# Kernel tuning notes

Hardware: AMD Instinct MI355X
Metric: run time of the kernel (lower is better)

Reference implementation:

```python
import jax, jax.numpy as jnp
import numpy as np

THRESHOLD_IOU = 0.8  # forward default in the original module


def setup_inputs() -> dict:
    key = jax.random.key(0)
    k1, k2, k3, k4 = jax.random.split(key, 4)
    N = M = 16
    H = W = 768
    # Binary masks (the original zeroes pixels to 0.0 and tests >0 via torch.where)
    masks_a = (jax.random.uniform(k1, (N, H, W)) > 0.6).astype(jnp.float32)
    masks_b = (jax.random.uniform(k2, (M, H, W)) > 0.6).astype(jnp.float32)
    # Make a few masks identical across labels so the IoU>threshold (suppression)
    # branch is exercised, not just the partial-overlap zeroing branch.
    masks_b = masks_b.at[:4].set(masks_a[:4])
    scores_a = jax.random.uniform(k3, (N,))
    scores_b = jax.random.uniform(k4, (M,))
    return {"masks_a": masks_a, "masks_b": masks_b,
            "scores_a": scores_a, "scores_b": scores_b}


def _overlap_filter(masks_a, masks_b, scores_a, scores_b, thr):
    # Sequential pairwise IoU + overlap zeroing, faithful to the original
    # nested product(enumerate(masks), enumerate(other_masks)) loop order
    # (i outer, j inner), where each pair sees masks already modified by
    # earlier pairs. Pruning ("keep") is applied after the loop; here it is
    # represented with static shapes as keep flags + zeroed-out rows.
    N, H, W = masks_a.shape
    M = masks_b.shape[0]
    P = H * W
    A0 = masks_a.reshape(N, P)
    B0 = masks_b.reshape(M, P)

    def body(carry, k):
        A, B, fi, fj = carry
        i = k // M
        j = k % M
        a = A[i]  # [P]
        b = B[j]  # [P]
        abin = a > 0
        bbin = b > 0
        inter = abin & bbin
        inter_sum = jnp.sum(inter.astype(jnp.float32))
        union_sum = jnp.sum((abin | bbin).astype(jnp.float32))
        iou = inter_sum / jnp.maximum(union_sum, 1.0)
        a_wins = scores_a[i] > scores_b[j]
        suppress = iou > thr                 # mark whole loser mask for removal
        zero_case = (iou > 0) & ~suppress    # zero overlapped pixels of loser
        b_new = jnp.where(zero_case & a_wins & inter, 0.0, b)
        a_new = jnp.where(zero_case & (~a_wins) & inter, 0.0, a)
        A = A.at[i].set(a_new)
        B = B.at[j].set(b_new)
        fj = fj.at[j].set(fj[j] | (suppress & a_wins))
        fi = fi.at[i].set(fi[i] | (suppress & ~a_wins))
        return (A, B, fi, fj), None

    fi0 = jnp.zeros(N, dtype=bool)
    fj0 = jnp.zeros(M, dtype=bool)
    (A, B, fi, fj), _ = jax.lax.scan(body, (A0, B0, fi0, fj0), jnp.arange(N * M))
    keep_a = ~fi
    keep_b = ~fj
    A = jnp.where(keep_a[:, None], A, 0.0)
    B = jnp.where(keep_b[:, None], B, 0.0)
    return A.reshape(N, H, W), B.reshape(M, H, W), keep_a, keep_b


def reference(masks_a, masks_b, scores_a, scores_b):
    return _overlap_filter(masks_a, masks_b, scores_a, scores_b, THRESHOLD_IOU)
```

## Files before the change

### kernel.cpp

```cpp
#include <hip/hip_runtime.h>
#include <stdint.h>

#define NM 16
#define HW_P 589824
#define WPM 18432
#define U8PM 9216
#define F4PM 147456
#define F4PT 2359296
#define PT 512
#define NG 8
#define U8PT 18

typedef unsigned long long u64;


__device__ __forceinline__ uint32_t spread4(uint32_t x) {
    uint32_t t = (x | (x << 12)) & 0x000F000Fu;
    t = (t | (t << 6)) & 0x03030303u;
    t = (t | (t << 3)) & 0x11111111u;
    return t;
}

__global__ __launch_bounds__(256) void binarize_kernel(
    const float* __restrict__ ma, const float* __restrict__ mb,
    uint32_t* __restrict__ bitsA, uint32_t* __restrict__ bitsB)
{
    int g = blockIdx.x * 256 + threadIdx.x;
    int tensor = (g >= F4PT);
    int lg = tensor ? (g - F4PT) : g;
    const float* src = tensor ? mb : ma;
    float4 v = ((const float4*)src)[lg];
    unsigned long long q0 = __ballot(v.x > 0.0f);
    unsigned long long q1 = __ballot(v.y > 0.0f);
    unsigned long long q2 = __ballot(v.z > 0.0f);
    unsigned long long q3 = __ballot(v.w > 0.0f);
    int lane = threadIdx.x & 63;
    if (lane < 8) {
        uint32_t wd = spread4((uint32_t)(q0 >> (8 * lane)) & 0xFFu)
                    | (spread4((uint32_t)(q1 >> (8 * lane)) & 0xFFu) << 1)
                    | (spread4((uint32_t)(q2 >> (8 * lane)) & 0xFFu) << 2)
                    | (spread4((uint32_t)(q3 >> (8 * lane)) & 0xFFu) << 3);
        uint32_t* bits = tensor ? bitsB : bitsA;
        bits[((lg & ~63) >> 3) + lane] = wd;
    }
}

__global__ __launch_bounds__(PT, 2) void pipeline_kernel(
    const float* __restrict__ sa, const float* __restrict__ sb,
    uint32_t* bitsA, uint32_t* bitsB, int* meta, u64* msg)
{
    int* flagsA = meta + 32;
    int* flagsB = meta + 48;
    unsigned* cons = (unsigned*)(meta + 64);
    unsigned* prodflag = (unsigned*)(meta + 96);

    const int g = blockIdx.x;
    const int tid = threadIdx.x;
    const int wave = tid >> 6, lane = tid & 63;
    const int c0 = 2 * g, c1 = 2 * g + 1;

    __shared__ int part[2][8][4];
    __shared__ unsigned smeta_s;

    u64* A8 = (u64*)bitsA;
    u64* B8 = (u64*)bitsB;

    u64 a[U8PT], b0[U8PT], b1[U8PT];
    int par = 0;

    int v0 = 0, v1 = 0;
#pragma unroll
    for (int w = 0; w < U8PT; ++w) {
        b0[w] = B8[(size_t)c0 * U8PM + tid + PT * w];
        b1[w] = B8[(size_t)c1 * U8PM + tid + PT * w];
        v0 += __popcll(b0[w]);
        v1 += __popcll(b1[w]);
    }
#pragma unroll
    for (int off = 32; off >= 1; off >>= 1) {
        v0 += __shfl_xor(v0, off); v1 += __shfl_xor(v1, off);
    }
    if (lane == 0) { part[par][wave][0] = v0; part[par][wave][1] = v1; }
    __syncthreads();
    int pcb0 = 0, pcb1 = 0;
#pragma unroll
    for (int w = 0; w < 8; ++w) { pcb0 += part[par][w][0]; pcb1 += part[par][w][1]; }
    par ^= 1;
    float sb0 = sb[c0], sb1 = sb[c1];
    int fb0 = 0, fb1 = 0;

    for (int t = 0; t < NM; ++t) {
        if (g > 0 && tid == 0) {
            unsigned v;
            while (!(v = __hip_atomic_load(&prodflag[(g - 1) * 16 + t],
                                           __ATOMIC_RELAXED, __HIP_MEMORY_SCOPE_AGENT)))
                __builtin_amdgcn_s_sleep(1);
            smeta_s = v;
        }
        if (g < NG - 1 && t >= 2 && tid == 64) {
            while (__hip_atomic_load(&cons[g], __ATOMIC_RELAXED,
                                     __HIP_MEMORY_SCOPE_AGENT) < (unsigned)(t - 1))
                __builtin_amdgcn_s_sleep(1);
        }
        __syncthreads();

        int pca, fa;
        if (g == 0) {
#pragma unroll
            for (int w = 0; w < U8PT; ++w)
                a[w] = A8[(size_t)t * U8PM + tid + PT * w];
            fa = 0; pca = 0;
        } else {
            unsigned v = smeta_s;
            pca = (int)((v >> 1) & 0xFFFFFu);
            fa  = (int)((v >> 21) & 1u);
            const u64* slot_in = msg + (size_t)((g - 1) * 2 + (t & 1)) * U8PM;
#pragma unroll
            for (int w = 0; w < U8PT; ++w)
                a[w] = __hip_atomic_load(&slot_in[tid + PT * w],
                                         __ATOMIC_RELAXED, __HIP_MEMORY_SCOPE_AGENT);
        }

        int i0 = 0, i1 = 0, it = 0, ip = 0;
#pragma unroll
        for (int w = 0; w < U8PT; ++w) {
            u64 ab0 = a[w] & b0[w];
            i0 += __popcll(ab0);
            i1 += __popcll(a[w] & b1[w]);
            it += __popcll(ab0 & b1[w]);
        }
        if (g == 0) {
#pragma unroll
            for (int w = 0; w < U8PT; ++w) ip += __popcll(a[w]);
        }
#pragma unroll
        for (int off = 32; off >= 1; off >>= 1) {
            i0 += __shfl_xor(i0, off); i1 += __shfl_xor(i1, off);
            it += __shfl_xor(it, off); ip += __shfl_xor(ip, off);
        }
        if (lane == 0) {
            part[par][wave][0] = i0; part[par][wave][1] = i1;
            part[par][wave][2] = it; part[par][wave][3] = ip;
        }
        __syncthreads();
        if (g > 0 && tid == 65)
            __hip_atomic_store(&cons[g - 1], (unsigned)(t + 1),
                               __ATOMIC_RELAXED, __HIP_MEMORY_SCOPE_AGENT);
        int I0 = 0, I1 = 0, T = 0, PC = 0;
#pragma unroll
        for (int w = 0; w < 8; ++w) {
            I0 += part[par][w][0]; I1 += part[par][w][1];
            T  += part[par][w][2]; PC += part[par][w][3];
        }
        par ^= 1;
        if (g == 0) pca = PC;

        float sai = sa[t];
        bool aupd = false;
        {
            int inter = I0;
            int uni = pca + pcb0 - inter;
            float iou = (float)inter / fmaxf((float)uni, 1.0f);
            bool aw = sai > sb0;
            if (iou > 0.8f) { if (aw) fb0 = 1; else fa = 1; }
            else if (inter > 0) {
                if (aw) {
                    pcb0 -= inter;
#pragma unroll
                    for (int w = 0; w < U8PT; ++w) b0[w] &= ~a[w];
                } else {
                    pca -= inter; aupd = true;
#pragma unroll
                    for (int w = 0; w < U8PT; ++w) a[w] &= ~b0[w];
                }
            }
        }
        {
            int inter = aupd ? (I1 - T) : I1;
            int uni = pca + pcb1 - inter;
            float iou = (float)inter / fmaxf((float)uni, 1.0f);
            bool aw = sai > sb1;
            if (iou > 0.8f) { if (aw) fb1 = 1; else fa = 1; }
            else if (inter > 0) {
                if (aw) {
                    pcb1 -= inter;
#pragma unroll
                    for (int w = 0; w < U8PT; ++w) b1[w] &= ~a[w];
                } else {
                    pca -= inter;
#pragma unroll
                    for (int w = 0; w < U8PT; ++w) a[w] &= ~b1[w];
                }
            }
        }

        if (g < NG - 1) {
            u64* slot_out = msg + (size_t)(g * 2 + (t & 1)) * U8PM;
#pragma unroll
            for (int w = 0; w < U8PT; ++w)
                __hip_atomic_store(&slot_out[tid + PT * w], a[w],
                                   __ATOMIC_RELAXED, __HIP_MEMORY_SCOPE_AGENT);
            __syncthreads();
            if (tid == 0)
                __hip_atomic_store(&prodflag[g * 16 + t],
                                   1u | ((unsigned)pca << 1) | ((unsigned)fa << 21),
                                   __ATOMIC_RELAXED, __HIP_MEMORY_SCOPE_AGENT);
        } else {
#pragma unroll
            for (int w = 0; w < U8PT; ++w)
                A8[(size_t)t * U8PM + tid + PT * w] = a[w];
            if (tid == 0) flagsA[t] = fa;
        }
    }
#pragma unroll
    for (int w = 0; w < U8PT; ++w) {
        B8[(size_t)c0 * U8PM + tid + PT * w] = b0[w];
        B8[(size_t)c1 * U8PM + tid + PT * w] = b1[w];
    }
    if (tid == 0) { flagsB[c0] = fb0; flagsB[c1] = fb1; }
}

__global__ __launch_bounds__(256) void expand_kernel(
    const uint32_t* __restrict__ bitsA, const uint32_t* __restrict__ bitsB,
    const int* __restrict__ meta, float* __restrict__ out)
{
    int g = blockIdx.x * 256 + threadIdx.x;
    int tensor = (g >= F4PT);
    int lg = tensor ? (g - F4PT) : g;
    const uint32_t* bits = tensor ? bitsB : bitsA;
    const int* flags = meta + (tensor ? 48 : 32);
    int m = lg / F4PM;
    bool keep = (flags[m] == 0);
    uint32_t wd = keep ? bits[lg >> 3] : 0u;
    int sh = (lg & 7) * 4;
    float4 o;
    o.x = ((wd >> (sh + 0)) & 1u) ? 1.0f : 0.0f;
    o.y = ((wd >> (sh + 1)) & 1u) ? 1.0f : 0.0f;
    o.z = ((wd >> (sh + 2)) & 1u) ? 1.0f : 0.0f;
    o.w = ((wd >> (sh + 3)) & 1u) ? 1.0f : 0.0f;
    ((float4*)out)[g] = o;
    if (g < 2 * NM) {
        const int* f = meta + 32;
        out[(size_t)2 * NM * HW_P + g] = f[g] ? 0.0f : 1.0f;
    }
}

extern "C" void kernel_launch(void* const* d_in, const int* in_sizes, int n_in,
                              void* d_out, int out_size, void* d_ws, size_t ws_size,
                              hipStream_t stream)
{
    const float* ma = (const float*)d_in[0];
    const float* mb = (const float*)d_in[1];
    const float* sa = (const float*)d_in[2];
    const float* sb = (const float*)d_in[3];
    float* out = (float*)d_out;
    char* ws = (char*)d_ws;

    uint32_t* bitsA = (uint32_t*)(ws);
    uint32_t* bitsB = (uint32_t*)(ws + 1179648);
    int* meta       = (int*)(ws + 2359296);
    u64* msg        = (u64*)(ws + 2360320);

    hipMemsetAsync(meta + 64, 0, 576, stream);

    binarize_kernel<<<18432, 256, 0, stream>>>(ma, mb, bitsA, bitsB);
    pipeline_kernel<<<NG, PT, 0, stream>>>(sa, sb, bitsA, bitsB, meta, msg);
    expand_kernel<<<18432, 256, 0, stream>>>(bitsA, bitsB, meta, out);
}
```

Before: 252.1 us.

## Deepen inter-block pipeline, drop memset, use nontemporal and 128-bit accesses

New measurement: 270.1 us. +7.1%, slower.

```diff
diff --git a/kernel.cpp b/kernel.cpp
--- a/kernel.cpp
+++ b/kernel.cpp
@@ -3,15 +3,14 @@
 
 #define NM 16
 #define HW_P 589824
-#define WPM 18432
 #define U8PM 9216
 #define F4PM 147456
 #define F4PT 2359296
 #define PT 512
 #define NG 8
-#define U8PT 18
 
 typedef unsigned long long u64;
+typedef float vf4 __attribute__((ext_vector_type(4)));
 
 
 __device__ __forceinline__ uint32_t spread4(uint32_t x) {
@@ -23,13 +22,15 @@
 
 __global__ __launch_bounds__(256) void binarize_kernel(
     const float* __restrict__ ma, const float* __restrict__ mb,
-    uint32_t* __restrict__ bitsA, uint32_t* __restrict__ bitsB)
+    uint32_t* __restrict__ bitsA, uint32_t* __restrict__ bitsB,
+    int* __restrict__ meta)
 {
+    if (blockIdx.x == 0) meta[threadIdx.x] = 0;
     int g = blockIdx.x * 256 + threadIdx.x;
     int tensor = (g >= F4PT);
     int lg = tensor ? (g - F4PT) : g;
     const float* src = tensor ? mb : ma;
-    float4 v = ((const float4*)src)[lg];
+    vf4 v = __builtin_nontemporal_load(((const vf4*)src) + lg);
     unsigned long long q0 = __ballot(v.x > 0.0f);
     unsigned long long q1 = __ballot(v.y > 0.0f);
     unsigned long long q2 = __ballot(v.z > 0.0f);
@@ -45,7 +46,7 @@
     }
 }
 
-__global__ __launch_bounds__(PT, 2) void pipeline_kernel(
+__global__ __launch_bounds__(PT, 1) void pipeline_kernel(
     const float* __restrict__ sa, const float* __restrict__ sb,
     uint32_t* bitsA, uint32_t* bitsB, int* meta, u64* msg)
 {
@@ -59,100 +60,108 @@
     const int wave = tid >> 6, lane = tid & 63;
     const int c0 = 2 * g, c1 = 2 * g + 1;
 
-    __shared__ int part[2][8][4];
+    __shared__ int part[8][4];
     __shared__ unsigned smeta_s;
 
     u64* A8 = (u64*)bitsA;
     u64* B8 = (u64*)bitsB;
 
-    u64 a[U8PT], b0[U8PT], b1[U8PT];
-    int par = 0;
-
+    u64 a[18], b0[18], b1[18];
+
+    const uint4* Bc0 = (const uint4*)(B8 + (size_t)c0 * U8PM);
+    const uint4* Bc1 = (const uint4*)(B8 + (size_t)c1 * U8PM);
+#pragma unroll
+    for (int w = 0; w < 9; ++w) {
+        uint4 q0 = Bc0[tid + PT * w];
+        uint4 q1 = Bc1[tid + PT * w];
+        b0[2 * w]     = ((u64)q0.y << 32) | q0.x;
+        b0[2 * w + 1] = ((u64)q0.w << 32) | q0.z;
+        b1[2 * w]     = ((u64)q1.y << 32) | q1.x;
+        b1[2 * w + 1] = ((u64)q1.w << 32) | q1.z;
+    }
     int v0 = 0, v1 = 0;
 #pragma unroll
-    for (int w = 0; w < U8PT; ++w) {
-        b0[w] = B8[(size_t)c0 * U8PM + tid + PT * w];
-        b1[w] = B8[(size_t)c1 * U8PM + tid + PT * w];
-        v0 += __popcll(b0[w]);
-        v1 += __popcll(b1[w]);
-    }
+    for (int w = 0; w < 18; ++w) { v0 += __popcll(b0[w]); v1 += __popcll(b1[w]); }
 #pragma unroll
     for (int off = 32; off >= 1; off >>= 1) {
         v0 += __shfl_xor(v0, off); v1 += __shfl_xor(v1, off);
     }
-    if (lane == 0) { part[par][wave][0] = v0; part[par][wave][1] = v1; }
+    if (lane == 0) { part[wave][0] = v0; part[wave][1] = v1; }
     __syncthreads();
     int pcb0 = 0, pcb1 = 0;
 #pragma unroll
-    for (int w = 0; w < 8; ++w) { pcb0 += part[par][w][0]; pcb1 += part[par][w][1]; }
-    par ^= 1;
+    for (int w = 0; w < 8; ++w) { pcb0 += part[wave ? 0 : 0][0], pcb0 = 0; break; }
+    pcb0 = 0; pcb1 = 0;
+#pragma unroll
+    for (int w = 0; w < 8; ++w) { pcb0 += part[w][0]; pcb1 += part[w][1]; }
+    if (g > 0 && tid == 64) {
+        unsigned v;
+        while (!(v = __hip_atomic_load(&prodflag[(g - 1) * 16 + 0],
+                                       __ATOMIC_RELAXED, __HIP_MEMORY_SCOPE_AGENT))) {}
+        smeta_s = v;
+    }
+    __syncthreads();
+    unsigned mv = smeta_s;
+
     float sb0 = sb[c0], sb1 = sb[c1];
     int fb0 = 0, fb1 = 0;
 
     for (int t = 0; t < NM; ++t) {
-        if (g > 0 && tid == 0) {
-            unsigned v;
-            while (!(v = __hip_atomic_load(&prodflag[(g - 1) * 16 + t],
-                                           __ATOMIC_RELAXED, __HIP_MEMORY_SCOPE_AGENT)))
-                __builtin_amdgcn_s_sleep(1);
-            smeta_s = v;
-        }
-        if (g < NG - 1 && t >= 2 && tid == 64) {
-            while (__hip_atomic_load(&cons[g], __ATOMIC_RELAXED,
-                                     __HIP_MEMORY_SCOPE_AGENT) < (unsigned)(t - 1))
-                __builtin_amdgcn_s_sleep(1);
-        }
-        __syncthreads();
-
         int pca, fa;
+        if (g == 0) { pca = 0; fa = 0; }
+        else { pca = (int)((mv >> 1) & 0xFFFFFu); fa = (int)((mv >> 21) & 1u); }
+
         if (g == 0) {
-#pragma unroll
-            for (int w = 0; w < U8PT; ++w)
-                a[w] = A8[(size_t)t * U8PM + tid + PT * w];
-            fa = 0; pca = 0;
+            const uint4* Ar = (const uint4*)(A8 + (size_t)t * U8PM);
+#pragma unroll
+            for (int w = 0; w < 9; ++w) {
+                uint4 q = Ar[tid + PT * w];
+                a[2 * w]     = ((u64)q.y << 32) | q.x;
+                a[2 * w + 1] = ((u64)q.w << 32) | q.z;
+            }
         } else {
-            unsigned v = smeta_s;
-            pca = (int)((v >> 1) & 0xFFFFFu);
-            fa  = (int)((v >> 21) & 1u);
-            const u64* slot_in = msg + (size_t)((g - 1) * 2 + (t & 1)) * U8PM;
-#pragma unroll
-            for (int w = 0; w < U8PT; ++w)
-                a[w] = __hip_atomic_load(&slot_in[tid + PT * w],
-                                         __ATOMIC_RELAXED, __HIP_MEMORY_SCOPE_AGENT);
-        }
-
-        int i0 = 0, i1 = 0, it = 0, ip = 0;
-#pragma unroll
-        for (int w = 0; w < U8PT; ++w) {
+            const u64* slot_in = msg + (size_t)((g - 1) * 4 + (t & 3)) * U8PM;
+#pragma unroll
+            for (int w = 0; w < 9; ++w) {
+                int base = 2 * tid + 1024 * w;
+                a[2 * w]     = __hip_atomic_load(&slot_in[base],
+                                __ATOMIC_RELAXED, __HIP_MEMORY_SCOPE_AGENT);
+                a[2 * w + 1] = __hip_atomic_load(&slot_in[base + 1],
+                                __ATOMIC_RELAXED, __HIP_MEMORY_SCOPE_AGENT);
+            }
+        }
+
+        int i0 = 0, i1 = 0, itr = 0, ipc = 0;
+#pragma unroll
+        for (int w = 0; w < 18; ++w) {
             u64 ab0 = a[w] & b0[w];
             i0 += __popcll(ab0);
             i1 += __popcll(a[w] & b1[w]);
-            it += __popcll(ab0 & b1[w]);
+            itr += __popcll(ab0 & b1[w]);
         }
         if (g == 0) {
 #pragma unroll
-            for (int w = 0; w < U8PT; ++w) ip += __popcll(a[w]);
+            for (int w = 0; w < 18; ++w) ipc += __popcll(a[w]);
         }
 #pragma unroll
         for (int off = 32; off >= 1; off >>= 1) {
             i0 += __shfl_xor(i0, off); i1 += __shfl_xor(i1, off);
-            it += __shfl_xor(it, off); ip += __shfl_xor(ip, off);
+            itr += __shfl_xor(itr, off); ipc += __shfl_xor(ipc, off);
         }
         if (lane == 0) {
-            part[par][wave][0] = i0; part[par][wave][1] = i1;
-            part[par][wave][2] = it; part[par][wave][3] = ip;
+            part[wave][0] = i0; part[wave][1] = i1;
+            part[wave][2] = itr; part[wave][3] = ipc;
         }
         __syncthreads();
-        if (g > 0 && tid == 65)
+        if (g > 0 && tid == 67)
             __hip_atomic_store(&cons[g - 1], (unsigned)(t + 1),
                                __ATOMIC_RELAXED, __HIP_MEMORY_SCOPE_AGENT);
         int I0 = 0, I1 = 0, T = 0, PC = 0;
 #pragma unroll
         for (int w = 0; w < 8; ++w) {
-            I0 += part[par][w][0]; I1 += part[par][w][1];
-            T  += part[par][w][2]; PC += part[par][w][3];
-        }
-        par ^= 1;
+            I0 += part[w][0]; I1 += part[w][1];
+            T  += part[w][2]; PC += part[w][3];
+        }
         if (g == 0) pca = PC;
 
         float sai = sa[t];
@@ -167,11 +176,11 @@
                 if (aw) {
                     pcb0 -= inter;
 #pragma unroll
-                    for (int w = 0; w < U8PT; ++w) b0[w] &= ~a[w];
+                    for (int w = 0; w < 18; ++w) b0[w] &= ~a[w];
                 } else {
                     pca -= inter; aupd = true;
 #pragma unroll
-                    for (int w = 0; w < U8PT; ++w) a[w] &= ~b0[w];
+                    for (int w = 0; w < 18; ++w) a[w] &= ~b0[w];
                 }
             }
         }
@@ -185,37 +194,66 @@
                 if (aw) {
                     pcb1 -= inter;
 #pragma unroll
-                    for (int w = 0; w < U8PT; ++w) b1[w] &= ~a[w];
+                    for (int w = 0; w < 18; ++w) b1[w] &= ~a[w];
                 } else {
                     pca -= inter;
 #pragma unroll
-                    for (int w = 0; w < U8PT; ++w) a[w] &= ~b1[w];
+                    for (int w = 0; w < 18; ++w) a[w] &= ~b1[w];
                 }
             }
         }
 
         if (g < NG - 1) {
-            u64* slot_out = msg + (size_t)(g * 2 + (t & 1)) * U8PM;
-#pragma unroll
-            for (int w = 0; w < U8PT; ++w)
-                __hip_atomic_store(&slot_out[tid + PT * w], a[w],
+            u64* slot_out = msg + (size_t)(g * 4 + (t & 3)) * U8PM;
+#pragma unroll
+            for (int w = 0; w < 9; ++w) {
+                int base = 2 * tid + 1024 * w;
+                __hip_atomic_store(&slot_out[base], a[2 * w],
                                    __ATOMIC_RELAXED, __HIP_MEMORY_SCOPE_AGENT);
-            __syncthreads();
-            if (tid == 0)
-                __hip_atomic_store(&prodflag[g * 16 + t],
-                                   1u | ((unsigned)pca << 1) | ((unsigned)fa << 21),
+                __hip_atomic_store(&slot_out[base + 1], a[2 * w + 1],
                                    __ATOMIC_RELAXED, __HIP_MEMORY_SCOPE_AGENT);
+            }
         } else {
-#pragma unroll
-            for (int w = 0; w < U8PT; ++w)
-                A8[(size_t)t * U8PM + tid + PT * w] = a[w];
+            uint4* Ar = (uint4*)(A8 + (size_t)t * U8PM);
+#pragma unroll
+            for (int w = 0; w < 9; ++w) {
+                uint4 q;
+                q.x = (uint32_t)a[2 * w];     q.y = (uint32_t)(a[2 * w] >> 32);
+                q.z = (uint32_t)a[2 * w + 1]; q.w = (uint32_t)(a[2 * w + 1] >> 32);
+                Ar[tid + PT * w] = q;
+            }
             if (tid == 0) flagsA[t] = fa;
         }
-    }
-#pragma unroll
-    for (int w = 0; w < U8PT; ++w) {
-        B8[(size_t)c0 * U8PM + tid + PT * w] = b0[w];
-        B8[(size_t)c1 * U8PM + tid + PT * w] = b1[w];
+
+        if (g > 0 && t + 1 < NM && tid == 64) {
+            unsigned v;
+            while (!(v = __hip_atomic_load(&prodflag[(g - 1) * 16 + t + 1],
+                                           __ATOMIC_RELAXED, __HIP_MEMORY_SCOPE_AGENT))) {}
+            smeta_s = v;
+        }
+        if (g < NG - 1 && t + 1 < NM && t + 1 >= 4 && tid == 65) {
+            while (__hip_atomic_load(&cons[g], __ATOMIC_RELAXED,
+                                     __HIP_MEMORY_SCOPE_AGENT) < (unsigned)(t - 2)) {}
+        }
+        __syncthreads();
+        if (g < NG - 1 && tid == 0)
+            __hip_atomic_store(&prodflag[g * 16 + t],
+                               1u | ((unsigned)pca << 1) | ((unsigned)fa << 21),
+                               __ATOMIC_RELAXED, __HIP_MEMORY_SCOPE_AGENT);
+        mv = smeta_s;
+    }
+
+    uint4* Wc0 = (uint4*)(B8 + (size_t)c0 * U8PM);
+    uint4* Wc1 = (uint4*)(B8 + (size_t)c1 * U8PM);
+#pragma unroll
+    for (int w = 0; w < 9; ++w) {
+        uint4 q0, q1;
+        q0.x = (uint32_t)b0[2 * w];     q0.y = (uint32_t)(b0[2 * w] >> 32);
+        q0.z = (uint32_t)b0[2 * w + 1]; q0.w = (uint32_t)(b0[2 * w + 1] >> 32);
+        q1.x = (uint32_t)b1[2 * w];     q1.y = (uint32_t)(b1[2 * w] >> 32);
+        q1.z = (uint32_t)b1[2 * w + 1]; q1.w = (uint32_t)(b1[2 * w + 1] >> 32);
+        Wc0[tid + PT * w] = q0;
+        Wc1[tid + PT * w] = q1;
     }
     if (tid == 0) { flagsB[c0] = fb0; flagsB[c1] = fb1; }
 }
@@ -233,12 +271,12 @@
     bool keep = (flags[m] == 0);
     uint32_t wd = keep ? bits[lg >> 3] : 0u;
     int sh = (lg & 7) * 4;
-    float4 o;
+    vf4 o;
     o.x = ((wd >> (sh + 0)) & 1u) ? 1.0f : 0.0f;
     o.y = ((wd >> (sh + 1)) & 1u) ? 1.0f : 0.0f;
     o.z = ((wd >> (sh + 2)) & 1u) ? 1.0f : 0.0f;
     o.w = ((wd >> (sh + 3)) & 1u) ? 1.0f : 0.0f;
-    ((float4*)out)[g] = o;
+    __builtin_nontemporal_store(o, ((vf4*)out) + g);
     if (g < 2 * NM) {
         const int* f = meta + 32;
         out[(size_t)2 * NM * HW_P + g] = f[g] ? 0.0f : 1.0f;
@@ -261,9 +299,7 @@
     int* meta       = (int*)(ws + 2359296);
     u64* msg        = (u64*)(ws + 2360320);
 
-    hipMemsetAsync(meta + 64, 0, 576, stream);
-
-    binarize_kernel<<<18432, 256, 0, stream>>>(ma, mb, bitsA, bitsB);
+    binarize_kernel<<<18432, 256, 0, stream>>>(ma, mb, bitsA, bitsB, meta);
     pipeline_kernel<<<NG, PT, 0, stream>>>(sa, sb, bitsA, bitsB, meta, msg);
     expand_kernel<<<18432, 256, 0, stream>>>(bitsA, bitsB, meta, out);
 }
```
